# Optimization experiments

Hardware: AMD Instinct MI355X
Metric: run time of the kernel (lower is better)

## Reference

```python
import jax, jax.numpy as jnp
import numpy as np
from jax import lax

# The 4 fixed 3x3 Sobel/diagonal kernels used by edge_conv2d128.
_SOBELS = jnp.asarray(np.stack([
    np.array([[-1, 0, 1], [-2, 0, 2], [-1, 0, 1]], dtype=np.float32),
    np.array([[ 1, 2, 1], [ 0, 0, 0], [-1,-2,-1]], dtype=np.float32),
    np.array([[ 2, 1, 0], [ 1, 0,-1], [ 0,-1,-2]], dtype=np.float32),
    np.array([[ 0,-1,-2], [ 1, 0,-1], [ 2, 1, 0]], dtype=np.float32),
], axis=0))  # [4, 3, 3]


def _edge_conv(x):
    """Faithful math of edge_conv2d128: 4 convs whose CxCx3x3 weights are the
    same Sobel kernel tiled over all in/out channels, abs each branch, sum.

    Because every (out_ch, in_ch) weight slice is identical, the tiled conv
    equals conv(sum_over_channels(x), sobel) broadcast to all C output
    channels -- we exploit that structure (identical math, one channel sum
    plus a single 4-output-channel 3x3 conv).
    """
    s = jnp.sum(x, axis=1, keepdims=True)              # [B, 1, H, W]
    k = _SOBELS[:, None, :, :]                          # [4, 1, 3, 3] OIHW
    e = lax.conv_general_dilated(
        s, k, window_strides=(1, 1), padding='SAME',
        dimension_numbers=('NCHW', 'OIHW', 'NCHW'))     # [B, 4, H, W]
    edge = jnp.sum(jnp.abs(e), axis=1, keepdims=True)   # [B, 1, H, W]
    return jnp.broadcast_to(edge, x.shape)              # [B, C, H, W]


def _maxpool2x2(x):
    # nn.MaxPool2d(kernel_size=2, stride=2)
    return lax.reduce_window(
        x, -jnp.inf, lax.max,
        window_dimensions=(1, 1, 2, 2),
        window_strides=(1, 1, 2, 2),
        padding='VALID')


def setup_inputs() -> dict:
    key = jax.random.key(0)
    x = jax.random.normal(key, (2, 128, 512, 512), dtype=jnp.float32)
    return {"x": x}


def reference(x) -> jnp.ndarray:
    # edge_conv2d128 (4 tiled Sobel convs + abs + sum) fused with downsample()
    return _maxpool2x2(_edge_conv(x))  # [B, C, H/2, W/2]
```

## Files before the change

kernel.cpp:

```cpp
#include <hip/hip_runtime.h>
#include <hip/hip_bf16.h>
#include <math.h>


#define N 2
#define C 128
#define H 512
#define W 512
#define HW (H * W)
#define PH 256
#define PW 256
#define PHW (PH * PW)

#define NHW4 (N * HW / 4)
#define SW 520
#define SR 514
#define SPLANE (SR * SW)

__global__ void __launch_bounds__(256) ksum_partial(const float* __restrict__ x,
                                                    float* __restrict__ part) {
    int idx = blockIdx.x * blockDim.x + threadIdx.x;
    int g   = blockIdx.y;
    int n   = idx >> 16;
    int sp  = idx & 65535;
    const float4* xp = (const float4*)(x + (size_t)n * C * HW) +
                       (size_t)g * 32 * (HW / 4) + sp;
    float4 acc = make_float4(0.f, 0.f, 0.f, 0.f);
#pragma unroll 8
    for (int c = 0; c < 32; ++c) {
        float4 v = xp[(size_t)c * (HW / 4)];
        acc.x += v.x; acc.y += v.y; acc.z += v.z; acc.w += v.w;
    }
    ((float4*)part)[(size_t)g * NHW4 + idx] = acc;
}

__global__ void __launch_bounds__(256) kreduce_pad(const float* __restrict__ part,
                                                   float* __restrict__ spad) {
    int idx = blockIdx.x * blockDim.x + threadIdx.x;
    int n  = idx >> 16;
    int sp = idx & 65535;
    int r  = sp / (W / 4);
    int c4 = (sp % (W / 4)) * 4;
    const float4* p = (const float4*)part;
    float4 a = p[idx];
    float4 b = p[idx + NHW4];
    float4 c = p[idx + 2 * NHW4];
    float4 d = p[idx + 3 * NHW4];
    float4 s;
    s.x = (a.x + b.x) + (c.x + d.x);
    s.y = (a.y + b.y) + (c.y + d.y);
    s.z = (a.z + b.z) + (c.z + d.z);
    s.w = (a.w + b.w) + (c.w + d.w);
    *(float4*)(spad + (size_t)n * SPLANE + (size_t)(r + 1) * SW + (c4 + 4)) = s;
}

__global__ void __launch_bounds__(256) kedge_pool_bcast(const float* __restrict__ spad,
                                                        float* __restrict__ out) {
    int idx = blockIdx.x * blockDim.x + threadIdx.x;
    int n   = idx / (PH * (PW / 4));
    int r   = idx % (PH * (PW / 4));
    int ph  = r / (PW / 4);
    int pw4 = (r % (PW / 4)) * 4;

    const float* sp = spad + (size_t)n * SPLANE + (size_t)(2 * ph) * SW + (2 * pw4 + 3);

    float v[4][10];
#pragma unroll
    for (int i = 0; i < 4; ++i)
#pragma unroll
        for (int j = 0; j < 10; ++j)
            v[i][j] = sp[(size_t)i * SW + j];

    float pool[4];
#pragma unroll
    for (int q = 0; q < 4; ++q) {
        float m = 0.f;
#pragma unroll
        for (int a = 0; a < 2; ++a) {
#pragma unroll
            for (int b = 0; b < 2; ++b) {
                int jb = 2 * q + b;
                float p00 = v[a    ][jb], p01 = v[a    ][jb + 1], p02 = v[a    ][jb + 2];
                float p10 = v[a + 1][jb],                         p12 = v[a + 1][jb + 2];
                float p20 = v[a + 2][jb], p21 = v[a + 2][jb + 1], p22 = v[a + 2][jb + 2];
                float e0 = -p00 + p02 - 2.f * p10 + 2.f * p12 - p20 + p22;
                float e1 =  p00 + 2.f * p01 + p02 - p20 - 2.f * p21 - p22;
                float e2 = 2.f * p00 + p01 + p10 - p12 - p21 - 2.f * p22;
                float e3 = -p01 - 2.f * p02 + p10 - p12 + 2.f * p20 + p21;
                float edge = fabsf(e0) + fabsf(e1) + fabsf(e2) + fabsf(e3);
                m = fmaxf(m, edge);
            }
        }
        pool[q] = m;
    }
    float4 pv = make_float4(pool[0], pool[1], pool[2], pool[3]);

    int cbase = blockIdx.y * 16;
    size_t base = (size_t)n * C * PHW + (size_t)cbase * PHW + (size_t)ph * PW + pw4;
#pragma unroll
    for (int c = 0; c < 16; ++c)
        *(float4*)(out + base + (size_t)c * PHW) = pv;
}

extern "C" void kernel_launch(void* const* d_in, const int* in_sizes, int n_in,
                              void* d_out, int out_size, void* d_ws, size_t ws_size,
                              hipStream_t stream) {
    const float* x = (const float*)d_in[0];
    float* out  = (float*)d_out;
    float* part = (float*)d_ws;
    float* spad = (float*)((char*)d_ws + (size_t)8 * 1024 * 1024);

    hipMemsetAsync(spad, 0, (size_t)N * SPLANE * sizeof(float), stream);

    ksum_partial<<<dim3(NHW4 / 256, 4), dim3(256), 0, stream>>>(x, part);

    kreduce_pad<<<dim3(NHW4 / 256), dim3(256), 0, stream>>>(part, spad);

    kedge_pool_bcast<<<dim3((N * PH * (PW / 4)) / 256, 8), dim3(256), 0, stream>>>(spad, out);
}
```

Measured before the change: 379.1 us.

## Fuse channel-sum partials and reduce into one kernel, use nontemporal loads/stores

Merges the four-way split channel sum and the separate reduce-and-pad kernel into one kernel in which each thread sums all 128 channels and writes straight into the padded plane. This removes a launch and the round trip of partial sums through global memory, but cuts the grid to a quarter of its former size (512 blocks of 256 threads) with longer serial dependent chains per thread. It also adds nontemporal hints on the streaming input loads and broadcast output stores to reduce cache pollution.

```diff
diff --git a/kernel.cpp b/kernel.cpp
--- a/kernel.cpp
+++ b/kernel.cpp
@@ -17,41 +17,23 @@
 #define SR 514
 #define SPLANE (SR * SW)
 
-__global__ void __launch_bounds__(256) ksum_partial(const float* __restrict__ x,
-                                                    float* __restrict__ part) {
+typedef float v4f __attribute__((ext_vector_type(4)));
+
+__global__ void __launch_bounds__(256) ksum_pad(const float* __restrict__ x,
+                                                float* __restrict__ spad) {
     int idx = blockIdx.x * blockDim.x + threadIdx.x;
-    int g   = blockIdx.y;
     int n   = idx >> 16;
     int sp  = idx & 65535;
-    const float4* xp = (const float4*)(x + (size_t)n * C * HW) +
-                       (size_t)g * 32 * (HW / 4) + sp;
-    float4 acc = make_float4(0.f, 0.f, 0.f, 0.f);
+    const v4f* xp = (const v4f*)(x + (size_t)n * C * HW) + sp;
+    v4f acc = (v4f)(0.f);
 #pragma unroll 8
-    for (int c = 0; c < 32; ++c) {
-        float4 v = xp[(size_t)c * (HW / 4)];
-        acc.x += v.x; acc.y += v.y; acc.z += v.z; acc.w += v.w;
+    for (int c = 0; c < C; ++c) {
+        v4f v = __builtin_nontemporal_load(&xp[(size_t)c * (HW / 4)]);
+        acc += v;
     }
-    ((float4*)part)[(size_t)g * NHW4 + idx] = acc;
-}
-
-__global__ void __launch_bounds__(256) kreduce_pad(const float* __restrict__ part,
-                                                   float* __restrict__ spad) {
-    int idx = blockIdx.x * blockDim.x + threadIdx.x;
-    int n  = idx >> 16;
-    int sp = idx & 65535;
-    int r  = sp / (W / 4);
-    int c4 = (sp % (W / 4)) * 4;
-    const float4* p = (const float4*)part;
-    float4 a = p[idx];
-    float4 b = p[idx + NHW4];
-    float4 c = p[idx + 2 * NHW4];
-    float4 d = p[idx + 3 * NHW4];
-    float4 s;
-    s.x = (a.x + b.x) + (c.x + d.x);
-    s.y = (a.y + b.y) + (c.y + d.y);
-    s.z = (a.z + b.z) + (c.z + d.z);
-    s.w = (a.w + b.w) + (c.w + d.w);
-    *(float4*)(spad + (size_t)n * SPLANE + (size_t)(r + 1) * SW + (c4 + 4)) = s;
+    int r  = sp >> 7;
+    int c4 = (sp & 127) << 2;
+    *(v4f*)(spad + (size_t)n * SPLANE + (size_t)(r + 1) * SW + (c4 + 4)) = acc;
 }
 
 __global__ void __launch_bounds__(256) kedge_pool_bcast(const float* __restrict__ spad,
@@ -93,13 +75,13 @@
         }
         pool[q] = m;
     }
-    float4 pv = make_float4(pool[0], pool[1], pool[2], pool[3]);
+    v4f pv = (v4f){pool[0], pool[1], pool[2], pool[3]};
 
     int cbase = blockIdx.y * 16;
     size_t base = (size_t)n * C * PHW + (size_t)cbase * PHW + (size_t)ph * PW + pw4;
 #pragma unroll
     for (int c = 0; c < 16; ++c)
-        *(float4*)(out + base + (size_t)c * PHW) = pv;
+        __builtin_nontemporal_store(pv, (v4f*)(out + base + (size_t)c * PHW));
 }
 
 extern "C" void kernel_launch(void* const* d_in, const int* in_sizes, int n_in,
@@ -107,14 +89,11 @@
                               hipStream_t stream) {
     const float* x = (const float*)d_in[0];
     float* out  = (float*)d_out;
-    float* part = (float*)d_ws;
-    float* spad = (float*)((char*)d_ws + (size_t)8 * 1024 * 1024);
+    float* spad = (float*)d_ws;
 
-    hipMemsetAsync(spad, 0, (size_t)N * SPLANE * sizeof(float), stream);
+    (void)hipMemsetAsync(spad, 0, (size_t)N * SPLANE * sizeof(float), stream);
 
-    ksum_partial<<<dim3(NHW4 / 256, 4), dim3(256), 0, stream>>>(x, part);
-
-    kreduce_pad<<<dim3(NHW4 / 256), dim3(256), 0, stream>>>(part, spad);
+    ksum_pad<<<dim3(NHW4 / 256), dim3(256), 0, stream>>>(x, spad);
 
     kedge_pool_bcast<<<dim3((N * PH * (PW / 4)) / 256, 8), dim3(256), 0, stream>>>(spad, out);
 }
```

New measurement: 352.2 us. -7.1%, faster.
